# Performance work log

Measured on AMD Instinct MI355X. Metric: run time of the kernel, lower is better.

## Reference

```python
import jax, jax.numpy as jnp
import numpy as np

B = 256      # number of graphs
IN = 128     # input_dim
FD = 256     # feature_dim (dims[1])
HID = 256    # hidden_dim of attention block (dims[2])
OUT = 128    # final output dim (dims[3])
TXT = 512    # text_emb_dim

LENGTHS = np.asarray(128 + (np.arange(B) % 256), dtype=np.int64)  # ragged lens 128..383
N = int(LENGTHS.sum())  # 65408 total nodes
LMAX = int(LENGTHS.max())  # 383


def setup_inputs() -> dict:
    key = jax.random.key(0)
    ks = jax.random.split(key, 16)
    s = 0.02
    return {
        "input": jax.random.normal(ks[0], (N, IN), jnp.float32),
        "text_emb": jax.random.normal(ks[1], (B, TXT), jnp.float32),
        "repeat_list": jnp.asarray(LENGTHS),
        # layer 0: Linear(IN -> FD)
        "W0": jax.random.normal(ks[2], (IN, FD), jnp.float32) * s,
        "b0": jax.random.normal(ks[3], (FD,), jnp.float32) * s,
        # cross-attention block params
        "Wq": jax.random.normal(ks[4], (TXT, FD), jnp.float32) * s,
        "bq": jax.random.normal(ks[5], (FD,), jnp.float32) * s,
        "Wk": jax.random.normal(ks[6], (FD, FD), jnp.float32) * s,
        "bk": jax.random.normal(ks[7], (FD,), jnp.float32) * s,
        "Wv": jax.random.normal(ks[8], (FD, FD), jnp.float32) * s,
        "bv": jax.random.normal(ks[9], (FD,), jnp.float32) * s,
        "Wo": jax.random.normal(ks[10], (FD, HID), jnp.float32) * s,
        "bo": jax.random.normal(ks[11], (HID,), jnp.float32) * s,
        # layer 2: Linear(HID -> OUT), last layer (no activation)
        "W2": jax.random.normal(ks[12], (HID, OUT), jnp.float32) * s,
        "b2": jax.random.normal(ks[13], (OUT,), jnp.float32) * s,
    }


def _cross_attention(h, text_emb, repeat_list, Wq, bq, Wk, bk, Wv, bv, Wo, bo):
    # h: [N, FD] packed ragged node features; repeat_list: [B] lengths (constant ints)
    n = h.shape[0]
    b = repeat_list.shape[0]
    fd = h.shape[1]
    # pad ragged -> [B, LMAX, FD] (pad value 0) + validity mask
    seg = jnp.repeat(jnp.arange(b), repeat_list, total_repeat_length=n)  # [N] graph id
    offsets = jnp.cumsum(repeat_list) - repeat_list                      # [B] start of each graph
    pos = jnp.arange(n) - offsets[seg]                                   # [N] within-graph pos
    padded = jnp.zeros((b, LMAX, fd), h.dtype).at[seg, pos].set(h)
    valid = jnp.arange(LMAX)[None, :] < repeat_list[:, None]             # [B, L]

    q = text_emb @ Wq + bq                              # [B, FD]
    k = (padded @ Wk + bk) * valid[..., None]           # masked_fill(mask==0, 0)
    v = (padded @ Wv + bv) * valid[..., None]

    # query is broadcast identically over the padded-length axis, so each row of the
    # [L, L] score matrix is the same vector: scores[b, j] = q[b] . k[b, j]
    scores = jnp.einsum('bf,bjf->bj', q, k)             # [B, L]
    scores = jnp.where(valid, scores, -jnp.inf)         # mask invalid columns j
    p = jax.nn.softmax(scores, axis=-1)                 # [B, L]
    # output = attention^T @ value with identical rows => out[b,j,:] = p[b,j] * sum_i v[b,i,:]
    v_sum = v.sum(axis=1)                               # [B, FD] (padded rows already zero)
    out_pad = p[..., None] * v_sum[:, None, :]          # [B, L, FD]
    out_nodes = out_pad[seg, pos]                       # unpad-concat -> [N, FD]
    return out_nodes @ Wo + bo                          # [N, HID]


def reference(input, text_emb, repeat_list, W0, b0, Wq, bq, Wk, bk, Wv, bv, Wo, bo, W2, b2):
    h = jax.nn.relu(input @ W0 + b0)                                     # layer 0 + relu
    h = _cross_attention(h, text_emb, repeat_list, Wq, bq, Wk, bk, Wv, bv, Wo, bo)
    h = jax.nn.relu(h)                                                   # layer 1 + relu
    return h @ W2 + b2                                                   # layer 2 (last, no act)
```

## Files before the change

kernel.cpp:

```cpp
#include <hip/hip_runtime.h>
#include <math.h>

#define B_G   256
#define IN_D  128
#define FD    256
#define HID   256
#define OUT_D 128
#define TXT   512
#define XKS   136
#define ZKS   264

typedef short bf16x8 __attribute__((ext_vector_type(8)));
typedef float f32x4  __attribute__((ext_vector_type(4)));

__device__ __forceinline__ unsigned bf_rne(float x) {
    unsigned u = __float_as_uint(x);
    u += 0x7fffu + ((u >> 16) & 1u);
    return u >> 16;
}
__device__ __forceinline__ float bf_to_f(unsigned h) {
    return __uint_as_float(h << 16);
}
__device__ __forceinline__ void split2(float a0, float a1, unsigned& hp, unsigned& lp) {
    unsigned h0 = bf_rne(a0), h1 = bf_rne(a1);
    float r0 = a0 - bf_to_f(h0), r1 = a1 - bf_to_f(h1);
    hp = h0 | (h1 << 16);
    lp = bf_rne(r0) | (bf_rne(r1) << 16);
}

__global__ __launch_bounds__(256) void k_prepA(
    const float* __restrict__ text_emb, const float* __restrict__ Wq,
    const float* __restrict__ bq, const float* __restrict__ Wk,
    const float* __restrict__ W0, const float* __restrict__ W2,
    const int* __restrict__ lens,
    float* __restrict__ qk, int* __restrict__ offsets, float* __restrict__ hsum,
    unsigned short* __restrict__ W0sH, unsigned short* __restrict__ W0sL,
    unsigned short* __restrict__ W2sH, unsigned short* __restrict__ W2sL)
{
    int blk = blockIdx.x, t = threadIdx.x;
    __shared__ float te[TXT];
    __shared__ float q[FD];
    __shared__ int   sc[B_G];

    if (blk < 256) {
        int b = blk;
        hsum[b * FD + t] = 0.f;
        for (int i = t; i < TXT; i += 256) te[i] = text_emb[(size_t)b * TXT + i];
        __syncthreads();
        float acc = bq[t];
        for (int k = 0; k < TXT; k++) acc = fmaf(te[k], Wq[k * FD + t], acc);
        q[t] = acc;
        __syncthreads();
        float a2 = 0.f;
        for (int f = 0; f < FD; f++) a2 = fmaf(Wk[t * FD + f], q[f], a2);
        qk[b * FD + t] = a2;
    } else if (blk < 264) {
        int e = (blk - 256) * 256 + t;
        if (e < 1024) {
            int kc = e >> 8, c = e & 255;
            size_t base = (size_t)(kc * 256 + c) * 32;
            for (int kk = 0; kk < 32; kk++) {
                float v = W0[(size_t)(kc * 32 + kk) * FD + c];
                unsigned h = bf_rne(v);
                float r = v - bf_to_f(h);
                W0sH[base + kk] = (unsigned short)h;
                W0sL[base + kk] = (unsigned short)bf_rne(r);
            }
        } else {
            int e2 = e - 1024;
            int kc = e2 >> 7, c = e2 & 127;
            size_t base = (size_t)(kc * 128 + c) * 32;
            for (int kk = 0; kk < 32; kk++) {
                float v = W2[(size_t)(kc * 32 + kk) * OUT_D + c];
                unsigned h = bf_rne(v);
                float r = v - bf_to_f(h);
                W2sH[base + kk] = (unsigned short)h;
                W2sL[base + kk] = (unsigned short)bf_rne(r);
            }
        }
    } else {
        sc[t] = lens[t];
        __syncthreads();
        for (int d = 1; d < 256; d <<= 1) {
            int v = (t >= d) ? sc[t - d] : 0;
            __syncthreads();
            sc[t] += v;
            __syncthreads();
        }
        offsets[t + 1] = sc[t];
        if (t == 0) offsets[0] = 0;
    }
}

__global__ __launch_bounds__(256, 2) void k_l0_mfma(
    const float* __restrict__ X,
    const unsigned short* __restrict__ W0sH, const unsigned short* __restrict__ W0sL,
    const float* __restrict__ b0, const float* __restrict__ qk,
    const int* __restrict__ offsets,
    float* __restrict__ scores, float* __restrict__ hsum)
{
    int b = blockIdx.y;
    int off = offsets[b], len = offsets[b + 1] - off;
    int n0 = blockIdx.x * 64;
    if (n0 >= len) return;
    int nvalid = min(64, len - n0);

    __shared__ __align__(16) unsigned short XsH[64 * XKS], XsL[64 * XKS];
    __shared__ float qks[FD];
    __shared__ float bsh[FD];
    __shared__ float red[4][64];

    int tid = threadIdx.x;
    int lane = tid & 63, w = tid >> 6;
    int ln = lane & 15, quad = lane >> 4;

    qks[tid] = qk[b * FD + tid];
    bsh[tid] = b0[tid];

    {
        int node_s = tid >> 2, ks = (tid & 3) * 32;
        const float* Xr = X + (size_t)(off + n0 + node_s) * IN_D + ks;
        float xv[32];
        if (node_s < nvalid) {
#pragma unroll
            for (int q2 = 0; q2 < 8; q2++) {
                float4 v = ((const float4*)Xr)[q2];
                xv[q2 * 4 + 0] = v.x; xv[q2 * 4 + 1] = v.y;
                xv[q2 * 4 + 2] = v.z; xv[q2 * 4 + 3] = v.w;
            }
        } else {
#pragma unroll
            for (int q2 = 0; q2 < 32; q2++) xv[q2] = 0.f;
        }
#pragma unroll
        for (int g = 0; g < 4; g++) {
            uint4 hq, lq;
            split2(xv[g * 8 + 0], xv[g * 8 + 1], hq.x, lq.x);
            split2(xv[g * 8 + 2], xv[g * 8 + 3], hq.y, lq.y);
            split2(xv[g * 8 + 4], xv[g * 8 + 5], hq.z, lq.z);
            split2(xv[g * 8 + 6], xv[g * 8 + 7], hq.w, lq.w);
            *(uint4*)&XsH[node_s * XKS + ks + g * 8] = hq;
            *(uint4*)&XsL[node_s * XKS + ks + g * 8] = lq;
        }
    }
    __syncthreads();

    f32x4 acc[4][4] = {};
#pragma unroll
    for (int kc = 0; kc < 4; kc++) {
        bf16x8 AH[4], AL[4], BH[4], BL[4];
#pragma unroll
        for (int i = 0; i < 4; i++) {
            AH[i] = *(const bf16x8*)&XsH[(16 * i + ln) * XKS + kc * 32 + quad * 8];
            AL[i] = *(const bf16x8*)&XsL[(16 * i + ln) * XKS + kc * 32 + quad * 8];
        }
#pragma unroll
        for (int j = 0; j < 4; j++) {
            int c = 64 * w + 16 * j + ln;
            size_t base = (size_t)(kc * 256 + c) * 32 + quad * 8;
            BH[j] = *(const bf16x8*)&W0sH[base];
            BL[j] = *(const bf16x8*)&W0sL[base];
        }
#pragma unroll
        for (int i = 0; i < 4; i++)
#pragma unroll
            for (int j = 0; j < 4; j++) {
                acc[i][j] = __builtin_amdgcn_mfma_f32_16x16x32_bf16(AH[i], BH[j], acc[i][j], 0, 0, 0);
                acc[i][j] = __builtin_amdgcn_mfma_f32_16x16x32_bf16(AH[i], BL[j], acc[i][j], 0, 0, 0);
                acc[i][j] = __builtin_amdgcn_mfma_f32_16x16x32_bf16(AL[i], BH[j], acc[i][j], 0, 0, 0);
            }
    }

    float sp[4][4];
    float cs[4] = {0.f, 0.f, 0.f, 0.f};
#pragma unroll
    for (int i = 0; i < 4; i++)
#pragma unroll
        for (int r = 0; r < 4; r++) sp[i][r] = 0.f;

#pragma unroll
    for (int i = 0; i < 4; i++)
#pragma unroll
        for (int j = 0; j < 4; j++) {
            int c = 64 * w + 16 * j + ln;
            float bb = bsh[c], qv = qks[c];
#pragma unroll
            for (int r = 0; r < 4; r++) {
                int node = 16 * i + 4 * quad + r;
                float h = acc[i][j][r] + bb;
                h = (h > 0.f && node < nvalid) ? h : 0.f;
                sp[i][r] = fmaf(h, qv, sp[i][r]);
                cs[j] += h;
            }
        }
#pragma unroll
    for (int i = 0; i < 4; i++)
#pragma unroll
        for (int r = 0; r < 4; r++) {
            float s = sp[i][r];
            s += __shfl_xor(s, 1); s += __shfl_xor(s, 2);
            s += __shfl_xor(s, 4); s += __shfl_xor(s, 8);
            sp[i][r] = s;
        }
    if (ln == 0) {
#pragma unroll
        for (int i = 0; i < 4; i++)
#pragma unroll
            for (int r = 0; r < 4; r++)
                red[w][16 * i + 4 * quad + r] = sp[i][r];
    }
#pragma unroll
    for (int j = 0; j < 4; j++) {
        float s = cs[j];
        s += __shfl_xor(s, 16); s += __shfl_xor(s, 32);
        if (quad == 0) atomicAdd(&hsum[b * FD + 64 * w + 16 * j + ln], s);
    }
    __syncthreads();
    if (tid < 64 && tid < nvalid)
        scores[off + n0 + tid] = red[0][tid] + red[1][tid] + red[2][tid] + red[3][tid];
}

__global__ __launch_bounds__(1024) void k_graph(
    const float* __restrict__ scores, const float* __restrict__ hsum,
    const float* __restrict__ Wv, const float* __restrict__ bv,
    const float* __restrict__ Wo, const int* __restrict__ offsets,
    float* __restrict__ wvec, float* __restrict__ smax, float* __restrict__ dinv)
{
    int b = blockIdx.x, tid = threadIdx.x;
    int t = tid & 255, g = tid >> 8;
    int off = offsets[b], len = offsets[b + 1] - off;
    __shared__ float redm[16], reds[16];
    __shared__ float hs[FD], vs[FD];
    __shared__ float part[4][FD];

    float m = -INFINITY;
    for (int i = tid; i < len; i += 1024) m = fmaxf(m, scores[off + i]);
    for (int d = 1; d < 64; d <<= 1) m = fmaxf(m, __shfl_xor(m, d));
    if ((tid & 63) == 0) redm[tid >> 6] = m;
    __syncthreads();
    m = -INFINITY;
#pragma unroll
    for (int k = 0; k < 16; k++) m = fmaxf(m, redm[k]);

    float s = 0.f;
    for (int i = tid; i < len; i += 1024) s += expf(scores[off + i] - m);
    for (int d = 1; d < 64; d <<= 1) s += __shfl_xor(s, d);
    if ((tid & 63) == 0) reds[tid >> 6] = s;
    if (g == 0) hs[t] = hsum[b * FD + t];
    __syncthreads();
    s = 0.f;
#pragma unroll
    for (int k = 0; k < 16; k++) s += reds[k];

    float acc = (g == 0) ? (float)len * bv[t] : 0.f;
    for (int f = 64 * g; f < 64 * g + 64; f++) acc = fmaf(hs[f], Wv[f * FD + t], acc);
    part[g][t] = acc;
    __syncthreads();
    if (g == 0) vs[t] = part[0][t] + part[1][t] + part[2][t] + part[3][t];
    __syncthreads();
    float a2 = 0.f;
    for (int f = 64 * g; f < 64 * g + 64; f++) a2 = fmaf(vs[f], Wo[f * HID + t], a2);
    part[g][t] = a2;
    __syncthreads();
    if (g == 0) wvec[b * HID + t] = part[0][t] + part[1][t] + part[2][t] + part[3][t];
    if (tid == 0) { smax[b] = m; dinv[b] = 1.0f / s; }
}

__global__ __launch_bounds__(256, 2) void k_fin_mfma(
    const float* __restrict__ scores, const float* __restrict__ wvec,
    const float* __restrict__ bo,
    const unsigned short* __restrict__ W2sH, const unsigned short* __restrict__ W2sL,
    const float* __restrict__ b2, const float* __restrict__ smax,
    const float* __restrict__ dinv, const int* __restrict__ offsets,
    float* __restrict__ Y)
{
    int b = blockIdx.y;
    int off = offsets[b], len = offsets[b + 1] - off;
    int n0 = blockIdx.x * 64;
    if (n0 >= len) return;
    int nvalid = min(64, len - n0);

    int tid = threadIdx.x;
    int lane = tid & 63, w = tid >> 6;
    int ln = lane & 15, quad = lane >> 4;

    __shared__ __align__(16) unsigned short ZsH[64 * ZKS], ZsL[64 * ZKS];
    __shared__ float ps[64];
    __shared__ float wsh[HID];
    __shared__ float bosh[HID];
    __shared__ float b2sh[OUT_D];

    wsh[tid] = wvec[b * HID + tid];
    bosh[tid] = bo[tid];
    if (tid < OUT_D) b2sh[tid] = b2[tid];
    if (tid < 64) {
        float p = 0.f;
        if (tid < nvalid) p = expf(scores[off + n0 + tid] - smax[b]) * dinv[b];
        ps[tid] = p;
    }
    __syncthreads();

    {
        int node_s = tid >> 2, ks = (tid & 3) * 64;
        float pn = ps[node_s];
#pragma unroll
        for (int g = 0; g < 8; g++) {
            uint4 hq, lq;
            int kb = ks + g * 8;
            float z0, z1;
            z0 = fmaxf(fmaf(pn, wsh[kb + 0], bosh[kb + 0]), 0.f);
            z1 = fmaxf(fmaf(pn, wsh[kb + 1], bosh[kb + 1]), 0.f);
            split2(z0, z1, hq.x, lq.x);
            z0 = fmaxf(fmaf(pn, wsh[kb + 2], bosh[kb + 2]), 0.f);
            z1 = fmaxf(fmaf(pn, wsh[kb + 3], bosh[kb + 3]), 0.f);
            split2(z0, z1, hq.y, lq.y);
            z0 = fmaxf(fmaf(pn, wsh[kb + 4], bosh[kb + 4]), 0.f);
            z1 = fmaxf(fmaf(pn, wsh[kb + 5], bosh[kb + 5]), 0.f);
            split2(z0, z1, hq.z, lq.z);
            z0 = fmaxf(fmaf(pn, wsh[kb + 6], bosh[kb + 6]), 0.f);
            z1 = fmaxf(fmaf(pn, wsh[kb + 7], bosh[kb + 7]), 0.f);
            split2(z0, z1, hq.w, lq.w);
            *(uint4*)&ZsH[node_s * ZKS + kb] = hq;
            *(uint4*)&ZsL[node_s * ZKS + kb] = lq;
        }
    }
    __syncthreads();

    f32x4 acc[4][2] = {};
#pragma unroll
    for (int kc = 0; kc < 8; kc++) {
        bf16x8 AH[4], AL[4], BH[2], BL[2];
#pragma unroll
        for (int i = 0; i < 4; i++) {
            AH[i] = *(const bf16x8*)&ZsH[(16 * i + ln) * ZKS + kc * 32 + quad * 8];
            AL[i] = *(const bf16x8*)&ZsL[(16 * i + ln) * ZKS + kc * 32 + quad * 8];
        }
#pragma unroll
        for (int j = 0; j < 2; j++) {
            int c = 32 * w + 16 * j + ln;
            size_t base = (size_t)(kc * 128 + c) * 32 + quad * 8;
            BH[j] = *(const bf16x8*)&W2sH[base];
            BL[j] = *(const bf16x8*)&W2sL[base];
        }
#pragma unroll
        for (int i = 0; i < 4; i++)
#pragma unroll
            for (int j = 0; j < 2; j++) {
                acc[i][j] = __builtin_amdgcn_mfma_f32_16x16x32_bf16(AH[i], BH[j], acc[i][j], 0, 0, 0);
                acc[i][j] = __builtin_amdgcn_mfma_f32_16x16x32_bf16(AH[i], BL[j], acc[i][j], 0, 0, 0);
                acc[i][j] = __builtin_amdgcn_mfma_f32_16x16x32_bf16(AL[i], BH[j], acc[i][j], 0, 0, 0);
            }
    }

#pragma unroll
    for (int i = 0; i < 4; i++)
#pragma unroll
        for (int j = 0; j < 2; j++) {
            int c = 32 * w + 16 * j + ln;
            float bb = b2sh[c];
#pragma unroll
            for (int r = 0; r < 4; r++) {
                int node = 16 * i + 4 * quad + r;
                if (node < nvalid)
                    Y[(size_t)(off + n0 + node) * OUT_D + c] = acc[i][j][r] + bb;
            }
        }
}

extern "C" void kernel_launch(void* const* d_in, const int* in_sizes, int n_in,
                              void* d_out, int out_size, void* d_ws, size_t ws_size,
                              hipStream_t stream)
{
    const float* X        = (const float*)d_in[0];
    const float* text_emb = (const float*)d_in[1];
    const int*   lens     = (const int*)d_in[2];
    const float* W0       = (const float*)d_in[3];
    const float* b0       = (const float*)d_in[4];
    const float* Wq       = (const float*)d_in[5];
    const float* bq       = (const float*)d_in[6];
    const float* Wk       = (const float*)d_in[7];
    const float* Wv       = (const float*)d_in[9];
    const float* bv       = (const float*)d_in[10];
    const float* Wo       = (const float*)d_in[11];
    const float* bo       = (const float*)d_in[12];
    const float* W2       = (const float*)d_in[13];
    const float* b2       = (const float*)d_in[14];
    float* Y = (float*)d_out;

    char* base = (char*)d_ws;
    size_t o = 0;
    int*   offsets = (int*)(base + o);            o += 1088;
    float* qkbuf   = (float*)(base + o);          o += 262144;
    float* wvec    = (float*)(base + o);          o += 262144;
    float* smaxb   = (float*)(base + o);          o += 1024;
    float* dinvb   = (float*)(base + o);          o += 1024;
    float* hsum    = (float*)(base + o);          o += 262144;
    float* scores  = (float*)(base + o);          o += 262144;
    unsigned short* W0sH = (unsigned short*)(base + o); o += 65536;
    unsigned short* W0sL = (unsigned short*)(base + o); o += 65536;
    unsigned short* W2sH = (unsigned short*)(base + o); o += 65536;
    unsigned short* W2sL = (unsigned short*)(base + o); o += 65536;

    k_prepA<<<265, 256, 0, stream>>>(text_emb, Wq, bq, Wk, W0, W2, lens,
                                     qkbuf, offsets, hsum, W0sH, W0sL, W2sH, W2sL);
    k_l0_mfma<<<dim3(6, B_G), 256, 0, stream>>>(X, W0sH, W0sL, b0, qkbuf, offsets, scores, hsum);
    k_graph<<<B_G, 1024, 0, stream>>>(scores, hsum, Wv, bv, Wo, offsets, wvec, smaxb, dinvb);
    k_fin_mfma<<<dim3(6, B_G), 256, 0, stream>>>(scores, wvec, bo, W2sH, W2sL, b2, smaxb, dinvb, offsets, Y);
}
```

Before: 199.2 us.

## Replace final MFMA GEMM with sorted breakpoint walk of piecewise-linear ReLU output

Within a graph, each node's hidden vector is relu(p*w + bo) with a per-graph w, so the final layer output is piecewise linear in the scalar p. The new final kernel sorts the ReLU breakpoints (-bo/w), buckets nodes by p, and walks the merged sequence from both ends, updating running slope and intercept vectors to produce Y = A*p + C + b2. This removes the per-node 256x128 matmul and the bf16 split of W2, at the cost of a serial per-graph walk, a bitonic sort, and one block per graph, which lowers parallelism. Accumulating slope and intercept in float across many breakpoints may shift rounding relative to the direct product.

After: 222.2 us. +11.5%, slower.

```diff
diff --git a/kernel.cpp b/kernel.cpp
--- a/kernel.cpp
+++ b/kernel.cpp
@@ -8,7 +8,6 @@
 #define OUT_D 128
 #define TXT   512
 #define XKS   136
-#define ZKS   264
 
 typedef short bf16x8 __attribute__((ext_vector_type(8)));
 typedef float f32x4  __attribute__((ext_vector_type(4)));
@@ -31,11 +30,9 @@
 __global__ __launch_bounds__(256) void k_prepA(
     const float* __restrict__ text_emb, const float* __restrict__ Wq,
     const float* __restrict__ bq, const float* __restrict__ Wk,
-    const float* __restrict__ W0, const float* __restrict__ W2,
-    const int* __restrict__ lens,
+    const float* __restrict__ W0, const int* __restrict__ lens,
     float* __restrict__ qk, int* __restrict__ offsets, float* __restrict__ hsum,
-    unsigned short* __restrict__ W0sH, unsigned short* __restrict__ W0sL,
-    unsigned short* __restrict__ W2sH, unsigned short* __restrict__ W2sL)
+    unsigned short* __restrict__ W0sH, unsigned short* __restrict__ W0sL)
 {
     int blk = blockIdx.x, t = threadIdx.x;
     __shared__ float te[TXT];
@@ -54,29 +51,16 @@
         float a2 = 0.f;
         for (int f = 0; f < FD; f++) a2 = fmaf(Wk[t * FD + f], q[f], a2);
         qk[b * FD + t] = a2;
-    } else if (blk < 264) {
+    } else if (blk < 260) {
         int e = (blk - 256) * 256 + t;
-        if (e < 1024) {
-            int kc = e >> 8, c = e & 255;
-            size_t base = (size_t)(kc * 256 + c) * 32;
-            for (int kk = 0; kk < 32; kk++) {
-                float v = W0[(size_t)(kc * 32 + kk) * FD + c];
-                unsigned h = bf_rne(v);
-                float r = v - bf_to_f(h);
-                W0sH[base + kk] = (unsigned short)h;
-                W0sL[base + kk] = (unsigned short)bf_rne(r);
-            }
-        } else {
-            int e2 = e - 1024;
-            int kc = e2 >> 7, c = e2 & 127;
-            size_t base = (size_t)(kc * 128 + c) * 32;
-            for (int kk = 0; kk < 32; kk++) {
-                float v = W2[(size_t)(kc * 32 + kk) * OUT_D + c];
-                unsigned h = bf_rne(v);
-                float r = v - bf_to_f(h);
-                W2sH[base + kk] = (unsigned short)h;
-                W2sL[base + kk] = (unsigned short)bf_rne(r);
-            }
+        int kc = e >> 8, c = e & 255;
+        size_t base = (size_t)(kc * 256 + c) * 32;
+        for (int kk = 0; kk < 32; kk++) {
+            float v = W0[(size_t)(kc * 32 + kk) * FD + c];
+            unsigned h = bf_rne(v);
+            float r = v - bf_to_f(h);
+            W0sH[base + kk] = (unsigned short)h;
+            W0sL[base + kk] = (unsigned short)bf_rne(r);
         }
     } else {
         sc[t] = lens[t];
@@ -266,105 +250,208 @@
     if (tid == 0) { smax[b] = m; dinv[b] = 1.0f / s; }
 }
 
-__global__ __launch_bounds__(256, 2) void k_fin_mfma(
+__global__ __launch_bounds__(256) void k_fin_walk(
     const float* __restrict__ scores, const float* __restrict__ wvec,
-    const float* __restrict__ bo,
-    const unsigned short* __restrict__ W2sH, const unsigned short* __restrict__ W2sL,
+    const float* __restrict__ bo, const float* __restrict__ W2,
     const float* __restrict__ b2, const float* __restrict__ smax,
     const float* __restrict__ dinv, const int* __restrict__ offsets,
     float* __restrict__ Y)
 {
-    int b = blockIdx.y;
+    int b = blockIdx.x, tid = threadIdx.x;
     int off = offsets[b], len = offsets[b + 1] - off;
-    int n0 = blockIdx.x * 64;
-    if (n0 >= len) return;
-    int nvalid = min(64, len - n0);
-
-    int tid = threadIdx.x;
-    int lane = tid & 63, w = tid >> 6;
-    int ln = lane & 15, quad = lane >> 4;
-
-    __shared__ __align__(16) unsigned short ZsH[64 * ZKS], ZsL[64 * ZKS];
-    __shared__ float ps[64];
-    __shared__ float wsh[HID];
-    __shared__ float bosh[HID];
-    __shared__ float b2sh[OUT_D];
-
-    wsh[tid] = wvec[b * HID + tid];
-    bosh[tid] = bo[tid];
-    if (tid < OUT_D) b2sh[tid] = b2[tid];
-    if (tid < 64) {
-        float p = 0.f;
-        if (tid < nvalid) p = expf(scores[off + n0 + tid] - smax[b]) * dinv[b];
-        ps[tid] = p;
-    }
-    __syncthreads();
-
+
+    __shared__ __align__(16) float W2s[HID][OUT_D];
+    __shared__ __align__(16) char scratch[10496];
+    __shared__ float tS[HID], dwS[HID], dbS[HID];
+    __shared__ int   kS[HID];
+    __shared__ float wS[HID], boS[HID];
+    __shared__ int   cnt[HID + 1];
+    __shared__ int   startS[HID + 2];
+    __shared__ float ps_s[384];
+    __shared__ int   nidx_s[384], bkt[384];
+    __shared__ float AINIT[4][OUT_D];
+    __shared__ float b2s[OUT_D];
+
+    unsigned long long* ebuf = (unsigned long long*)scratch;
+    float* ptmp  = (float*)scratch;
+    int*   rtmp  = (int*)(scratch + 1536);
+    float4* part4 = (float4*)scratch;
+    float* opA = (float*)scratch;
+    float* opB = (float*)(scratch + 2624);
+    int*   opN = (int*)(scratch + 5248);
+    int*   opK = (int*)(scratch + 7872);
+
+    float m = smax[b], di = dinv[b];
+
+    float wreg = wvec[b * HID + tid];
+    float breg = bo[tid];
+    wS[tid] = wreg; boS[tid] = breg;
+    if (tid < OUT_D) b2s[tid] = b2[tid];
     {
-        int node_s = tid >> 2, ks = (tid & 3) * 64;
-        float pn = ps[node_s];
-#pragma unroll
-        for (int g = 0; g < 8; g++) {
-            uint4 hq, lq;
-            int kb = ks + g * 8;
-            float z0, z1;
-            z0 = fmaxf(fmaf(pn, wsh[kb + 0], bosh[kb + 0]), 0.f);
-            z1 = fmaxf(fmaf(pn, wsh[kb + 1], bosh[kb + 1]), 0.f);
-            split2(z0, z1, hq.x, lq.x);
-            z0 = fmaxf(fmaf(pn, wsh[kb + 2], bosh[kb + 2]), 0.f);
-            z1 = fmaxf(fmaf(pn, wsh[kb + 3], bosh[kb + 3]), 0.f);
-            split2(z0, z1, hq.y, lq.y);
-            z0 = fmaxf(fmaf(pn, wsh[kb + 4], bosh[kb + 4]), 0.f);
-            z1 = fmaxf(fmaf(pn, wsh[kb + 5], bosh[kb + 5]), 0.f);
-            split2(z0, z1, hq.z, lq.z);
-            z0 = fmaxf(fmaf(pn, wsh[kb + 6], bosh[kb + 6]), 0.f);
-            z1 = fmaxf(fmaf(pn, wsh[kb + 7], bosh[kb + 7]), 0.f);
-            split2(z0, z1, hq.w, lq.w);
-            *(uint4*)&ZsH[node_s * ZKS + kb] = hq;
-            *(uint4*)&ZsL[node_s * ZKS + kb] = lq;
-        }
-    }
-    __syncthreads();
-
-    f32x4 acc[4][2] = {};
-#pragma unroll
-    for (int kc = 0; kc < 8; kc++) {
-        bf16x8 AH[4], AL[4], BH[2], BL[2];
-#pragma unroll
-        for (int i = 0; i < 4; i++) {
-            AH[i] = *(const bf16x8*)&ZsH[(16 * i + ln) * ZKS + kc * 32 + quad * 8];
-            AL[i] = *(const bf16x8*)&ZsL[(16 * i + ln) * ZKS + kc * 32 + quad * 8];
-        }
-#pragma unroll
-        for (int j = 0; j < 2; j++) {
-            int c = 32 * w + 16 * j + ln;
-            size_t base = (size_t)(kc * 128 + c) * 32 + quad * 8;
-            BH[j] = *(const bf16x8*)&W2sH[base];
-            BL[j] = *(const bf16x8*)&W2sL[base];
-        }
-#pragma unroll
-        for (int i = 0; i < 4; i++)
-#pragma unroll
-            for (int j = 0; j < 2; j++) {
-                acc[i][j] = __builtin_amdgcn_mfma_f32_16x16x32_bf16(AH[i], BH[j], acc[i][j], 0, 0, 0);
-                acc[i][j] = __builtin_amdgcn_mfma_f32_16x16x32_bf16(AH[i], BL[j], acc[i][j], 0, 0, 0);
-                acc[i][j] = __builtin_amdgcn_mfma_f32_16x16x32_bf16(AL[i], BH[j], acc[i][j], 0, 0, 0);
-            }
-    }
-
-#pragma unroll
-    for (int i = 0; i < 4; i++)
-#pragma unroll
-        for (int j = 0; j < 2; j++) {
-            int c = 32 * w + 16 * j + ln;
-            float bb = b2sh[c];
-#pragma unroll
-            for (int r = 0; r < 4; r++) {
-                int node = 16 * i + 4 * quad + r;
-                if (node < nvalid)
-                    Y[(size_t)(off + n0 + node) * OUT_D + c] = acc[i][j][r] + bb;
-            }
-        }
+        const float4* gv = (const float4*)W2;
+        float4* lv = (float4*)&W2s[0][0];
+        for (int i = tid; i < HID * OUT_D / 4; i += 256) lv[i] = gv[i];
+    }
+
+    bool isev = (wreg > 0.f && breg < 0.f) || (wreg < 0.f && breg > 0.f);
+    float tk = isev ? (-breg / wreg) : INFINITY;
+    ebuf[tid] = ((unsigned long long)__float_as_uint(tk) << 32) | (unsigned)tid;
+    int nE = __syncthreads_count(isev);
+    __syncthreads();
+
+    for (int ksz = 2; ksz <= 256; ksz <<= 1) {
+        for (int js = ksz >> 1; js > 0; js >>= 1) {
+            int ixj = tid ^ js;
+            if (ixj > tid) {
+                unsigned long long a = ebuf[tid], bb2 = ebuf[ixj];
+                bool sw = ((tid & ksz) == 0) ? (a > bb2) : (a < bb2);
+                if (sw) { ebuf[tid] = bb2; ebuf[ixj] = a; }
+            }
+            __syncthreads();
+        }
+    }
+
+    {
+        unsigned long long e = ebuf[tid];
+        int k = (int)(unsigned)(e & 0xffffffffULL);
+        unsigned tb = (unsigned)(e >> 32);
+        bool real = (tb & 0x7f800000u) != 0x7f800000u;
+        tS[tid] = __uint_as_float(tb);
+        float wv = wS[k], bv = boS[k];
+        dwS[tid] = real ? fabsf(wv) : 0.f;
+        dbS[tid] = real ? -fabsf(bv) : 0.f;
+        kS[tid] = k;
+        cnt[tid] = 0;
+        if (tid == 0) cnt[256] = 0;
+    }
+    __syncthreads();
+
+    for (int n = tid; n < len; n += 256) {
+        float p = expf(scores[off + n] - m) * di;
+        int r = 0;
+#pragma unroll
+        for (int st = 128; st > 0; st >>= 1)
+            if (tS[r + st - 1] < p) r += st;
+        ptmp[n] = p; rtmp[n] = r;
+        atomicAdd(&cnt[r], 1);
+    }
+    __syncthreads();
+
+    for (int d = 1; d < 256; d <<= 1) {
+        int v = (tid >= d) ? cnt[tid - d] : 0;
+        __syncthreads();
+        cnt[tid] += v;
+        __syncthreads();
+    }
+    startS[tid + 1] = cnt[tid];
+    if (tid == 0) { startS[0] = 0; startS[257] = len; }
+    __syncthreads();
+
+    cnt[tid] = startS[tid];
+    if (tid == 0) cnt[256] = startS[256];
+    __syncthreads();
+    for (int n = tid; n < len; n += 256) {
+        int r = rtmp[n];
+        float p = ptmp[n];
+        int slot = atomicAdd(&cnt[r], 1);
+        ps_s[slot] = p; nidx_s[slot] = n; bkt[slot] = r;
+    }
+    __syncthreads();
+
+    {
+        int cI = tid & 127, hh = tid >> 7;
+        float A0 = 0.f, C0 = 0.f, AE = 0.f, CE = 0.f;
+        for (int k = hh * 128; k < hh * 128 + 128; ++k) {
+            float vv = W2s[k][cI];
+            float wv = wS[k], bv = boS[k];
+            bool ini = (bv > 0.f) || (bv == 0.f && wv > 0.f);
+            bool pos = (wv > 0.f);
+            A0 = fmaf(ini ? wv : 0.f, vv, A0);
+            C0 = fmaf(ini ? bv : 0.f, vv, C0);
+            AE = fmaf(pos ? wv : 0.f, vv, AE);
+            CE = fmaf((pos || (wv == 0.f && bv > 0.f)) ? bv : 0.f, vv, CE);
+        }
+        part4[hh * 128 + cI] = make_float4(A0, C0, AE, CE);
+    }
+    __syncthreads();
+    if (tid < 128) {
+        float4 x = part4[tid], y = part4[128 + tid];
+        AINIT[0][tid] = x.x + y.x;
+        AINIT[1][tid] = x.y + y.y;
+        AINIT[2][tid] = x.z + y.z;
+        AINIT[3][tid] = x.w + y.w;
+    }
+    __syncthreads();
+
+    int L = len + nE;
+    int Lpad = (L + 7) & ~7;
+    for (int s = tid; s < len; s += 256) {
+        int j = bkt[s];
+        int pos = s + j;
+        opA[pos] = ps_s[s]; opB[pos] = 0.f; opN[pos] = nidx_s[s]; opK[pos] = 0;
+    }
+    for (int j = tid; j < nE; j += 256) {
+        int pos = startS[j + 1] + j;
+        opA[pos] = dwS[j]; opB[pos] = dbS[j]; opN[pos] = -1; opK[pos] = kS[j];
+    }
+    for (int i = L + tid; i < Lpad + 8; i += 256) {
+        opA[i] = 0.f; opB[i] = 0.f; opN[i] = -1; opK[i] = 0;
+    }
+    __syncthreads();
+
+    {
+        int lane = tid & 63;
+        int c = ((tid >> 6) & 1) * 64 + lane;
+        float b2v = b2s[c];
+        float* Yb = Y + (size_t)off * OUT_D + c;
+        int P = (L >> 1) & ~7;
+        float rA[8], rB[8], rV[4]; int rN[8], rK[8];
+        float A, C;
+        if (tid < 128) {
+            A = AINIT[0][c]; C = AINIT[1][c];
+#pragma unroll
+            for (int u = 0; u < 8; ++u) { rA[u]=opA[u]; rB[u]=opB[u]; rN[u]=opN[u]; rK[u]=opK[u]; }
+#pragma unroll
+            for (int u = 0; u < 4; ++u) rV[u] = W2s[rK[u]][c];
+            for (int i0 = 0; i0 < P; i0 += 8) {
+#pragma unroll
+                for (int u = 0; u < 8; ++u) {
+                    int i = i0 + u;
+                    float aI = rA[u], bI = rB[u], vv = rV[u & 3];
+                    int nI = rN[u];
+                    rA[u] = opA[i + 8]; rB[u] = opB[i + 8];
+                    rN[u] = opN[i + 8]; rK[u] = opK[i + 8];
+                    int kpf = (u < 4) ? rK[u + 4] : rK[u - 4];
+                    rV[u & 3] = W2s[kpf][c];
+                    if (nI >= 0) Yb[(size_t)nI * OUT_D] = fmaf(aI, A, C) + b2v;
+                    else { A = fmaf(aI, vv, A); C = fmaf(bI, vv, C); }
+                }
+            }
+        } else {
+            A = AINIT[2][c]; C = AINIT[3][c];
+            int base = Lpad - 8;
+#pragma unroll
+            for (int u = 0; u < 8; ++u) { rA[u]=opA[base+u]; rB[u]=opB[base+u]; rN[u]=opN[base+u]; rK[u]=opK[base+u]; }
+#pragma unroll
+            for (int u = 0; u < 4; ++u) rV[u] = W2s[rK[u + 4]][c];
+            for (int i0 = base; i0 >= P; i0 -= 8) {
+#pragma unroll
+                for (int uu = 0; uu < 8; ++uu) {
+                    int u = 7 - uu;
+                    int i = i0 + u;
+                    float aI = rA[u], bI = rB[u], vv = rV[u & 3];
+                    int nI = rN[u];
+                    int ipf = i - 8;
+                    rA[u] = opA[ipf]; rB[u] = opB[ipf];
+                    rN[u] = opN[ipf]; rK[u] = opK[ipf];
+                    int kpf = (u >= 4) ? rK[u - 4] : rK[u + 4];
+                    rV[u & 3] = W2s[kpf][c];
+                    if (nI >= 0) Yb[(size_t)nI * OUT_D] = fmaf(aI, A, C) + b2v;
+                    else { A = fmaf(-aI, vv, A); C = fmaf(-bI, vv, C); }
+                }
+            }
+        }
+    }
 }
 
 extern "C" void kernel_launch(void* const* d_in, const int* in_sizes, int n_in,
@@ -398,12 +485,10 @@
     float* scores  = (float*)(base + o);          o += 262144;
     unsigned short* W0sH = (unsigned short*)(base + o); o += 65536;
     unsigned short* W0sL = (unsigned short*)(base + o); o += 65536;
-    unsigned short* W2sH = (unsigned short*)(base + o); o += 65536;
-    unsigned short* W2sL = (unsigned short*)(base + o); o += 65536;
-
-    k_prepA<<<265, 256, 0, stream>>>(text_emb, Wq, bq, Wk, W0, W2, lens,
-                                     qkbuf, offsets, hsum, W0sH, W0sL, W2sH, W2sL);
+
+    k_prepA<<<261, 256, 0, stream>>>(text_emb, Wq, bq, Wk, W0, lens,
+                                     qkbuf, offsets, hsum, W0sH, W0sL);
     k_l0_mfma<<<dim3(6, B_G), 256, 0, stream>>>(X, W0sH, W0sL, b0, qkbuf, offsets, scores, hsum);
     k_graph<<<B_G, 1024, 0, stream>>>(scores, hsum, Wv, bv, Wo, offsets, wvec, smaxb, dinvb);
-    k_fin_mfma<<<dim3(6, B_G), 256, 0, stream>>>(scores, wvec, bo, W2sH, W2sL, b2, smaxb, dinvb, offsets, Y);
-}
+    k_fin_walk<<<B_G, 256, 0, stream>>>(scores, wvec, bo, W2, b2, smaxb, dinvb, offsets, Y);
+}
```

## Replace final MFMA GEMM with sorted breakpoint walk over piecewise-linear ReLU

Applied to the files above, without the earlier changes.

Each node's hidden vector is relu(p*w + bo), which is piecewise linear in the scalar p. The final layer is therefore computed by sorting ReLU breakpoints and nodes by p and walking them in order while updating running A and C accumulators, so each output is a single fma instead of a 256-deep GEMM row. This removes the split-bf16 MFMA work and the W2 preprocessing. In exchange it adds sorting, scans, atomics and a sequential walk per segment, and it changes the floating-point summation order.

Result: no change. 202.3 us (+1.5%).

```diff
diff --git a/kernel.cpp b/kernel.cpp
--- a/kernel.cpp
+++ b/kernel.cpp
@@ -8,7 +8,6 @@
 #define OUT_D 128
 #define TXT   512
 #define XKS   136
-#define ZKS   264
 
 typedef short bf16x8 __attribute__((ext_vector_type(8)));
 typedef float f32x4  __attribute__((ext_vector_type(4)));
@@ -31,11 +30,9 @@
 __global__ __launch_bounds__(256) void k_prepA(
     const float* __restrict__ text_emb, const float* __restrict__ Wq,
     const float* __restrict__ bq, const float* __restrict__ Wk,
-    const float* __restrict__ W0, const float* __restrict__ W2,
-    const int* __restrict__ lens,
+    const float* __restrict__ W0, const int* __restrict__ lens,
     float* __restrict__ qk, int* __restrict__ offsets, float* __restrict__ hsum,
-    unsigned short* __restrict__ W0sH, unsigned short* __restrict__ W0sL,
-    unsigned short* __restrict__ W2sH, unsigned short* __restrict__ W2sL)
+    unsigned short* __restrict__ W0sH, unsigned short* __restrict__ W0sL)
 {
     int blk = blockIdx.x, t = threadIdx.x;
     __shared__ float te[TXT];
@@ -54,29 +51,16 @@
         float a2 = 0.f;
         for (int f = 0; f < FD; f++) a2 = fmaf(Wk[t * FD + f], q[f], a2);
         qk[b * FD + t] = a2;
-    } else if (blk < 264) {
+    } else if (blk < 260) {
         int e = (blk - 256) * 256 + t;
-        if (e < 1024) {
-            int kc = e >> 8, c = e & 255;
-            size_t base = (size_t)(kc * 256 + c) * 32;
-            for (int kk = 0; kk < 32; kk++) {
-                float v = W0[(size_t)(kc * 32 + kk) * FD + c];
-                unsigned h = bf_rne(v);
-                float r = v - bf_to_f(h);
-                W0sH[base + kk] = (unsigned short)h;
-                W0sL[base + kk] = (unsigned short)bf_rne(r);
-            }
-        } else {
-            int e2 = e - 1024;
-            int kc = e2 >> 7, c = e2 & 127;
-            size_t base = (size_t)(kc * 128 + c) * 32;
-            for (int kk = 0; kk < 32; kk++) {
-                float v = W2[(size_t)(kc * 32 + kk) * OUT_D + c];
-                unsigned h = bf_rne(v);
-                float r = v - bf_to_f(h);
-                W2sH[base + kk] = (unsigned short)h;
-                W2sL[base + kk] = (unsigned short)bf_rne(r);
-            }
+        int kc = e >> 8, c = e & 255;
+        size_t base = (size_t)(kc * 256 + c) * 32;
+        for (int kk = 0; kk < 32; kk++) {
+            float v = W0[(size_t)(kc * 32 + kk) * FD + c];
+            unsigned h = bf_rne(v);
+            float r = v - bf_to_f(h);
+            W0sH[base + kk] = (unsigned short)h;
+            W0sL[base + kk] = (unsigned short)bf_rne(r);
         }
     } else {
         sc[t] = lens[t];
@@ -266,105 +250,176 @@
     if (tid == 0) { smax[b] = m; dinv[b] = 1.0f / s; }
 }
 
-__global__ __launch_bounds__(256, 2) void k_fin_mfma(
+__global__ __launch_bounds__(1024) void k_fin_walk(
     const float* __restrict__ scores, const float* __restrict__ wvec,
-    const float* __restrict__ bo,
-    const unsigned short* __restrict__ W2sH, const unsigned short* __restrict__ W2sL,
+    const float* __restrict__ bo, const float* __restrict__ W2,
     const float* __restrict__ b2, const float* __restrict__ smax,
     const float* __restrict__ dinv, const int* __restrict__ offsets,
     float* __restrict__ Y)
 {
-    int b = blockIdx.y;
+    int b = blockIdx.x, tid = threadIdx.x;
     int off = offsets[b], len = offsets[b + 1] - off;
-    int n0 = blockIdx.x * 64;
-    if (n0 >= len) return;
-    int nvalid = min(64, len - n0);
-
-    int tid = threadIdx.x;
-    int lane = tid & 63, w = tid >> 6;
-    int ln = lane & 15, quad = lane >> 4;
-
-    __shared__ __align__(16) unsigned short ZsH[64 * ZKS], ZsL[64 * ZKS];
-    __shared__ float ps[64];
-    __shared__ float wsh[HID];
-    __shared__ float bosh[HID];
-    __shared__ float b2sh[OUT_D];
-
-    wsh[tid] = wvec[b * HID + tid];
-    bosh[tid] = bo[tid];
-    if (tid < OUT_D) b2sh[tid] = b2[tid];
+
+    __shared__ float tOrig[256];
+    __shared__ float tS[256], dwS[256], dbS[256];
+    __shared__ int   kS[256];
+    __shared__ float wS[256], boS[256];
+    __shared__ int   cnt[257], startS[257];
+    __shared__ float A0s[OUT_D], C0s[OUT_D], b2s[OUT_D];
+    __shared__ float segA[8][OUT_D], segC[8][OUT_D];
+    __shared__ __align__(16) char ops_raw[656 * 16];
+    float* opA = (float*)ops_raw;
+    float* opB = (float*)(ops_raw + 2624);
+    int*   opN = (int*)(ops_raw + 5248);
+    int*   opK = (int*)(ops_raw + 7872);
+
+    float m = smax[b], di = dinv[b];
+
+    bool real = false;
+    if (tid < 256) {
+        float wv = wvec[b * HID + tid];
+        float bv = bo[tid];
+        wS[tid] = wv; boS[tid] = bv;
+        bool isev = (wv > 0.f && bv < 0.f) || (wv < 0.f && bv > 0.f);
+        float tk = isev ? (-bv / wv) : INFINITY;
+        real = isev && (tk < INFINITY);
+        tOrig[tid] = real ? tk : INFINITY;
+        cnt[tid] = 0;
+        if (tid == 0) cnt[256] = 0;
+    }
+    if (tid < OUT_D) b2s[tid] = b2[tid];
+    __syncthreads();
+
+    if (tid < 256) {
+        float tk = tOrig[tid];
+        int r = 0;
+        for (int j = 0; j < 256; j++) {
+            float tj = tOrig[j];
+            r += (tj < tk || (tj == tk && j < tid)) ? 1 : 0;
+        }
+        tS[r] = tk;
+        kS[r] = tid;
+        float wv = wS[tid], bv = boS[tid];
+        dwS[r] = real ? fabsf(wv) : 0.f;
+        dbS[r] = real ? -fabsf(bv) : 0.f;
+    }
+    {
+        int q = tid >> 7, c = tid & 127;
+        float pa = 0.f, pc = 0.f;
+        for (int k = q * 32; k < q * 32 + 32; ++k) {
+            float v = W2[(size_t)k * OUT_D + c];
+            float wv = wS[k], bv = boS[k];
+            bool ini = (bv > 0.f) || (bv == 0.f && wv > 0.f);
+            pa = fmaf(ini ? wv : 0.f, v, pa);
+            pc = fmaf(ini ? bv : 0.f, v, pc);
+        }
+        segA[q][c] = pa; segC[q][c] = pc;
+    }
+    int nE = __syncthreads_count(real);
+
+    float p_n = 0.f; int r_n = 0;
+    if (tid < len) {
+        p_n = expf(scores[off + tid] - m) * di;
+        int r = 0;
+#pragma unroll
+        for (int st = 128; st > 0; st >>= 1)
+            if (tS[r + st - 1] < p_n) r += st;
+        r_n = r;
+        atomicAdd(&cnt[r], 1);
+    }
+    if (tid < OUT_D) {
+        float sa = 0.f, sc2 = 0.f;
+#pragma unroll
+        for (int q = 0; q < 8; q++) { sa += segA[q][tid]; sc2 += segC[q][tid]; }
+        A0s[tid] = sa; C0s[tid] = sc2;
+    }
+    __syncthreads();
+
     if (tid < 64) {
-        float p = 0.f;
-        if (tid < nvalid) p = expf(scores[off + n0 + tid] - smax[b]) * dinv[b];
-        ps[tid] = p;
-    }
-    __syncthreads();
-
+        int l = tid;
+        int v0 = cnt[4 * l], v1 = cnt[4 * l + 1], v2 = cnt[4 * l + 2], v3 = cnt[4 * l + 3];
+        int s0 = v0, s1 = s0 + v1, s2 = s1 + v2, s3 = s2 + v3;
+        int run = s3;
+#pragma unroll
+        for (int d = 1; d < 64; d <<= 1) {
+            int t2 = __shfl_up(run, d);
+            if (l >= d) run += t2;
+        }
+        int base = run - s3;
+        startS[4 * l + 0] = base;      cnt[4 * l + 0] = base;
+        startS[4 * l + 1] = base + s0; cnt[4 * l + 1] = base + s0;
+        startS[4 * l + 2] = base + s1; cnt[4 * l + 2] = base + s1;
+        startS[4 * l + 3] = base + s2; cnt[4 * l + 3] = base + s2;
+        if (l == 63) { startS[256] = base + s3; cnt[256] = base + s3; }
+    }
+    __syncthreads();
+
+    int L    = len + nE;
+    int Lpad = (L + 7) & ~7;
+    int Lseg = ((Lpad + 63) >> 6) << 3;
+
+    if (tid < len) {
+        int slot = atomicAdd(&cnt[r_n], 1);
+        int pos = slot + r_n;
+        opA[pos] = p_n; opB[pos] = 0.f; opN[pos] = tid; opK[pos] = 0;
+    }
+    if (tid < nE) {
+        int pos = startS[tid + 1] + tid;
+        opA[pos] = dwS[tid]; opB[pos] = dbS[tid]; opN[pos] = -1; opK[pos] = kS[tid];
+    }
+    for (int i = L + tid; i < 648; i += 1024) {
+        opA[i] = 0.f; opB[i] = 0.f; opN[i] = -1; opK[i] = 0;
+    }
+    __syncthreads();
+
+    int s = tid >> 7, c = tid & 127;
     {
-        int node_s = tid >> 2, ks = (tid & 3) * 64;
-        float pn = ps[node_s];
-#pragma unroll
-        for (int g = 0; g < 8; g++) {
-            uint4 hq, lq;
-            int kb = ks + g * 8;
-            float z0, z1;
-            z0 = fmaxf(fmaf(pn, wsh[kb + 0], bosh[kb + 0]), 0.f);
-            z1 = fmaxf(fmaf(pn, wsh[kb + 1], bosh[kb + 1]), 0.f);
-            split2(z0, z1, hq.x, lq.x);
-            z0 = fmaxf(fmaf(pn, wsh[kb + 2], bosh[kb + 2]), 0.f);
-            z1 = fmaxf(fmaf(pn, wsh[kb + 3], bosh[kb + 3]), 0.f);
-            split2(z0, z1, hq.y, lq.y);
-            z0 = fmaxf(fmaf(pn, wsh[kb + 4], bosh[kb + 4]), 0.f);
-            z1 = fmaxf(fmaf(pn, wsh[kb + 5], bosh[kb + 5]), 0.f);
-            split2(z0, z1, hq.z, lq.z);
-            z0 = fmaxf(fmaf(pn, wsh[kb + 6], bosh[kb + 6]), 0.f);
-            z1 = fmaxf(fmaf(pn, wsh[kb + 7], bosh[kb + 7]), 0.f);
-            split2(z0, z1, hq.w, lq.w);
-            *(uint4*)&ZsH[node_s * ZKS + kb] = hq;
-            *(uint4*)&ZsL[node_s * ZKS + kb] = lq;
-        }
-    }
-    __syncthreads();
-
-    f32x4 acc[4][2] = {};
-#pragma unroll
-    for (int kc = 0; kc < 8; kc++) {
-        bf16x8 AH[4], AL[4], BH[2], BL[2];
-#pragma unroll
-        for (int i = 0; i < 4; i++) {
-            AH[i] = *(const bf16x8*)&ZsH[(16 * i + ln) * ZKS + kc * 32 + quad * 8];
-            AL[i] = *(const bf16x8*)&ZsL[(16 * i + ln) * ZKS + kc * 32 + quad * 8];
-        }
-#pragma unroll
-        for (int j = 0; j < 2; j++) {
-            int c = 32 * w + 16 * j + ln;
-            size_t base = (size_t)(kc * 128 + c) * 32 + quad * 8;
-            BH[j] = *(const bf16x8*)&W2sH[base];
-            BL[j] = *(const bf16x8*)&W2sL[base];
-        }
-#pragma unroll
-        for (int i = 0; i < 4; i++)
-#pragma unroll
-            for (int j = 0; j < 2; j++) {
-                acc[i][j] = __builtin_amdgcn_mfma_f32_16x16x32_bf16(AH[i], BH[j], acc[i][j], 0, 0, 0);
-                acc[i][j] = __builtin_amdgcn_mfma_f32_16x16x32_bf16(AH[i], BL[j], acc[i][j], 0, 0, 0);
-                acc[i][j] = __builtin_amdgcn_mfma_f32_16x16x32_bf16(AL[i], BH[j], acc[i][j], 0, 0, 0);
+        int iBeg = s * Lseg, iEnd = iBeg + Lseg;
+        int lo = 0, hi = nE;
+        while (lo < hi) {
+            int mid = (lo + hi) >> 1;
+            if (startS[mid + 1] + mid < iBeg) lo = mid + 1; else hi = mid;
+        }
+        float dA = 0.f, dC = 0.f;
+        for (int j = lo; j < nE && (startS[j + 1] + j) < iEnd; ++j) {
+            float v = W2[(size_t)kS[j] * OUT_D + c];
+            dA = fmaf(dwS[j], v, dA);
+            dC = fmaf(dbS[j], v, dC);
+        }
+        segA[s][c] = dA; segC[s][c] = dC;
+    }
+    __syncthreads();
+
+    {
+        float A = A0s[c], C = C0s[c];
+        for (int s2 = 0; s2 < s; ++s2) { A += segA[s2][c]; C += segC[s2][c]; }
+        float b2v = b2s[c];
+        float* Yb = Y + (size_t)off * OUT_D + c;
+        int i0 = s * Lseg;
+
+        float rA[8], rB[8], rV[8]; int rN[8], rK[8];
+#pragma unroll
+        for (int u = 0; u < 8; ++u) {
+            rA[u] = opA[i0 + u]; rB[u] = opB[i0 + u];
+            rN[u] = opN[i0 + u]; rK[u] = opK[i0 + u];
+        }
+#pragma unroll
+        for (int u = 0; u < 8; ++u) rV[u] = W2[(size_t)rK[u] * OUT_D + c];
+
+        for (int i0w = i0; i0w < i0 + Lseg; i0w += 8) {
+#pragma unroll
+            for (int u = 0; u < 8; ++u) {
+                int i = i0w + u;
+                float aI = rA[u], bI = rB[u], vv = rV[u];
+                int nI = rN[u];
+                rA[u] = opA[i + 8]; rB[u] = opB[i + 8];
+                rN[u] = opN[i + 8]; rK[u] = opK[i + 8];
+                rV[u] = W2[(size_t)rK[u] * OUT_D + c];
+                if (nI >= 0) Yb[(size_t)nI * OUT_D] = fmaf(aI, A, C) + b2v;
+                else { A = fmaf(aI, vv, A); C = fmaf(bI, vv, C); }
             }
-    }
-
-#pragma unroll
-    for (int i = 0; i < 4; i++)
-#pragma unroll
-        for (int j = 0; j < 2; j++) {
-            int c = 32 * w + 16 * j + ln;
-            float bb = b2sh[c];
-#pragma unroll
-            for (int r = 0; r < 4; r++) {
-                int node = 16 * i + 4 * quad + r;
-                if (node < nvalid)
-                    Y[(size_t)(off + n0 + node) * OUT_D + c] = acc[i][j][r] + bb;
-            }
-        }
+        }
+    }
 }
 
 extern "C" void kernel_launch(void* const* d_in, const int* in_sizes, int n_in,
@@ -398,12 +453,10 @@
     float* scores  = (float*)(base + o);          o += 262144;
     unsigned short* W0sH = (unsigned short*)(base + o); o += 65536;
     unsigned short* W0sL = (unsigned short*)(base + o); o += 65536;
-    unsigned short* W2sH = (unsigned short*)(base + o); o += 65536;
-    unsigned short* W2sL = (unsigned short*)(base + o); o += 65536;
-
-    k_prepA<<<265, 256, 0, stream>>>(text_emb, Wq, bq, Wk, W0, W2, lens,
-                                     qkbuf, offsets, hsum, W0sH, W0sL, W2sH, W2sL);
+
+    k_prepA<<<261, 256, 0, stream>>>(text_emb, Wq, bq, Wk, W0, lens,
+                                     qkbuf, offsets, hsum, W0sH, W0sL);
     k_l0_mfma<<<dim3(6, B_G), 256, 0, stream>>>(X, W0sH, W0sL, b0, qkbuf, offsets, scores, hsum);
     k_graph<<<B_G, 1024, 0, stream>>>(scores, hsum, Wv, bv, Wo, offsets, wvec, smaxb, dinvb);
-    k_fin_mfma<<<dim3(6, B_G), 256, 0, stream>>>(scores, wvec, bo, W2sH, W2sL, b2, smaxb, dinvb, offsets, Y);
-}
+    k_fin_walk<<<B_G, 1024, 0, stream>>>(scores, wvec, bo, W2, b2, smaxb, dinvb, offsets, Y);
+}
```

## Raise occupancy of MFMA kernels by cutting registers and halving LDS tile

Applied to the files above, without the earlier changes.

Both MFMA kernels now declare launch bounds of four blocks per CU instead of two. In the layer-0 kernel, X is streamed in float4 pairs instead of a 32-float register array, and B fragments are loaded per column tile right before use rather than held all at once. In the final kernel, the K=256 staging buffer is split into two K=128 halves that reuse one smaller LDS tile, which adds an extra barrier per half. The goal is more resident waves to hide memory latency, at the risk of spills or less instruction-level overlap.

Result: no change. 201.0 us (+0.9%).

```diff
diff --git a/kernel.cpp b/kernel.cpp
--- a/kernel.cpp
+++ b/kernel.cpp
@@ -8,7 +8,6 @@
 #define OUT_D 128
 #define TXT   512
 #define XKS   136
-#define ZKS   264
 
 typedef short bf16x8 __attribute__((ext_vector_type(8)));
 typedef float f32x4  __attribute__((ext_vector_type(4)));
@@ -92,7 +91,7 @@
     }
 }
 
-__global__ __launch_bounds__(256, 2) void k_l0_mfma(
+__global__ __launch_bounds__(256, 4) void k_l0_mfma(
     const float* __restrict__ X,
     const unsigned short* __restrict__ W0sH, const unsigned short* __restrict__ W0sL,
     const float* __restrict__ b0, const float* __restrict__ qk,
@@ -119,26 +118,18 @@
 
     {
         int node_s = tid >> 2, ks = (tid & 3) * 32;
-        const float* Xr = X + (size_t)(off + n0 + node_s) * IN_D + ks;
-        float xv[32];
-        if (node_s < nvalid) {
-#pragma unroll
-            for (int q2 = 0; q2 < 8; q2++) {
-                float4 v = ((const float4*)Xr)[q2];
-                xv[q2 * 4 + 0] = v.x; xv[q2 * 4 + 1] = v.y;
-                xv[q2 * 4 + 2] = v.z; xv[q2 * 4 + 3] = v.w;
-            }
-        } else {
-#pragma unroll
-            for (int q2 = 0; q2 < 32; q2++) xv[q2] = 0.f;
-        }
+        const float4* Xr4 = (const float4*)(X + (size_t)(off + n0 + node_s) * IN_D + ks);
+        bool v = (node_s < nvalid);
 #pragma unroll
         for (int g = 0; g < 4; g++) {
+            float4 a, c4;
+            if (v) { a = Xr4[2 * g]; c4 = Xr4[2 * g + 1]; }
+            else   { a = make_float4(0.f, 0.f, 0.f, 0.f); c4 = a; }
             uint4 hq, lq;
-            split2(xv[g * 8 + 0], xv[g * 8 + 1], hq.x, lq.x);
-            split2(xv[g * 8 + 2], xv[g * 8 + 3], hq.y, lq.y);
-            split2(xv[g * 8 + 4], xv[g * 8 + 5], hq.z, lq.z);
-            split2(xv[g * 8 + 6], xv[g * 8 + 7], hq.w, lq.w);
+            split2(a.x,  a.y,  hq.x, lq.x);
+            split2(a.z,  a.w,  hq.y, lq.y);
+            split2(c4.x, c4.y, hq.z, lq.z);
+            split2(c4.z, c4.w, hq.w, lq.w);
             *(uint4*)&XsH[node_s * XKS + ks + g * 8] = hq;
             *(uint4*)&XsL[node_s * XKS + ks + g * 8] = lq;
         }
@@ -148,7 +139,7 @@
     f32x4 acc[4][4] = {};
 #pragma unroll
     for (int kc = 0; kc < 4; kc++) {
-        bf16x8 AH[4], AL[4], BH[4], BL[4];
+        bf16x8 AH[4], AL[4];
 #pragma unroll
         for (int i = 0; i < 4; i++) {
             AH[i] = *(const bf16x8*)&XsH[(16 * i + ln) * XKS + kc * 32 + quad * 8];
@@ -158,17 +149,15 @@
         for (int j = 0; j < 4; j++) {
             int c = 64 * w + 16 * j + ln;
             size_t base = (size_t)(kc * 256 + c) * 32 + quad * 8;
-            BH[j] = *(const bf16x8*)&W0sH[base];
-            BL[j] = *(const bf16x8*)&W0sL[base];
-        }
-#pragma unroll
-        for (int i = 0; i < 4; i++)
-#pragma unroll
-            for (int j = 0; j < 4; j++) {
-                acc[i][j] = __builtin_amdgcn_mfma_f32_16x16x32_bf16(AH[i], BH[j], acc[i][j], 0, 0, 0);
-                acc[i][j] = __builtin_amdgcn_mfma_f32_16x16x32_bf16(AH[i], BL[j], acc[i][j], 0, 0, 0);
-                acc[i][j] = __builtin_amdgcn_mfma_f32_16x16x32_bf16(AL[i], BH[j], acc[i][j], 0, 0, 0);
-            }
+            bf16x8 BH = *(const bf16x8*)&W0sH[base];
+            bf16x8 BL = *(const bf16x8*)&W0sL[base];
+#pragma unroll
+            for (int i = 0; i < 4; i++) {
+                acc[i][j] = __builtin_amdgcn_mfma_f32_16x16x32_bf16(AH[i], BH, acc[i][j], 0, 0, 0);
+                acc[i][j] = __builtin_amdgcn_mfma_f32_16x16x32_bf16(AH[i], BL, acc[i][j], 0, 0, 0);
+                acc[i][j] = __builtin_amdgcn_mfma_f32_16x16x32_bf16(AL[i], BH, acc[i][j], 0, 0, 0);
+            }
+        }
     }
 
     float sp[4][4];
@@ -266,7 +255,7 @@
     if (tid == 0) { smax[b] = m; dinv[b] = 1.0f / s; }
 }
 
-__global__ __launch_bounds__(256, 2) void k_fin_mfma(
+__global__ __launch_bounds__(256, 4) void k_fin_mfma(
     const float* __restrict__ scores, const float* __restrict__ wvec,
     const float* __restrict__ bo,
     const unsigned short* __restrict__ W2sH, const unsigned short* __restrict__ W2sL,
@@ -284,7 +273,7 @@
     int lane = tid & 63, w = tid >> 6;
     int ln = lane & 15, quad = lane >> 4;
 
-    __shared__ __align__(16) unsigned short ZsH[64 * ZKS], ZsL[64 * ZKS];
+    __shared__ __align__(16) unsigned short ZsH[64 * XKS], ZsL[64 * XKS];
     __shared__ float ps[64];
     __shared__ float wsh[HID];
     __shared__ float bosh[HID];
@@ -300,56 +289,60 @@
     }
     __syncthreads();
 
-    {
-        int node_s = tid >> 2, ks = (tid & 3) * 64;
-        float pn = ps[node_s];
-#pragma unroll
-        for (int g = 0; g < 8; g++) {
-            uint4 hq, lq;
-            int kb = ks + g * 8;
-            float z0, z1;
-            z0 = fmaxf(fmaf(pn, wsh[kb + 0], bosh[kb + 0]), 0.f);
-            z1 = fmaxf(fmaf(pn, wsh[kb + 1], bosh[kb + 1]), 0.f);
-            split2(z0, z1, hq.x, lq.x);
-            z0 = fmaxf(fmaf(pn, wsh[kb + 2], bosh[kb + 2]), 0.f);
-            z1 = fmaxf(fmaf(pn, wsh[kb + 3], bosh[kb + 3]), 0.f);
-            split2(z0, z1, hq.y, lq.y);
-            z0 = fmaxf(fmaf(pn, wsh[kb + 4], bosh[kb + 4]), 0.f);
-            z1 = fmaxf(fmaf(pn, wsh[kb + 5], bosh[kb + 5]), 0.f);
-            split2(z0, z1, hq.z, lq.z);
-            z0 = fmaxf(fmaf(pn, wsh[kb + 6], bosh[kb + 6]), 0.f);
-            z1 = fmaxf(fmaf(pn, wsh[kb + 7], bosh[kb + 7]), 0.f);
-            split2(z0, z1, hq.w, lq.w);
-            *(uint4*)&ZsH[node_s * ZKS + kb] = hq;
-            *(uint4*)&ZsL[node_s * ZKS + kb] = lq;
-        }
-    }
-    __syncthreads();
-
     f32x4 acc[4][2] = {};
-#pragma unroll
-    for (int kc = 0; kc < 8; kc++) {
-        bf16x8 AH[4], AL[4], BH[2], BL[2];
-#pragma unroll
-        for (int i = 0; i < 4; i++) {
-            AH[i] = *(const bf16x8*)&ZsH[(16 * i + ln) * ZKS + kc * 32 + quad * 8];
-            AL[i] = *(const bf16x8*)&ZsL[(16 * i + ln) * ZKS + kc * 32 + quad * 8];
-        }
-#pragma unroll
-        for (int j = 0; j < 2; j++) {
-            int c = 32 * w + 16 * j + ln;
-            size_t base = (size_t)(kc * 128 + c) * 32 + quad * 8;
-            BH[j] = *(const bf16x8*)&W2sH[base];
-            BL[j] = *(const bf16x8*)&W2sL[base];
-        }
-#pragma unroll
-        for (int i = 0; i < 4; i++)
+    int node_s = tid >> 2, ks = (tid & 3) * 32;
+
+#pragma unroll
+    for (int h = 0; h < 2; h++) {
+        if (h) __syncthreads();
+        {
+            float pn = ps[node_s];
+            int kg0 = h * 128 + ks;
+#pragma unroll
+            for (int g = 0; g < 4; g++) {
+                uint4 hq, lq;
+                int kb = kg0 + g * 8;
+                float z0, z1;
+                z0 = fmaxf(fmaf(pn, wsh[kb + 0], bosh[kb + 0]), 0.f);
+                z1 = fmaxf(fmaf(pn, wsh[kb + 1], bosh[kb + 1]), 0.f);
+                split2(z0, z1, hq.x, lq.x);
+                z0 = fmaxf(fmaf(pn, wsh[kb + 2], bosh[kb + 2]), 0.f);
+                z1 = fmaxf(fmaf(pn, wsh[kb + 3], bosh[kb + 3]), 0.f);
+                split2(z0, z1, hq.y, lq.y);
+                z0 = fmaxf(fmaf(pn, wsh[kb + 4], bosh[kb + 4]), 0.f);
+                z1 = fmaxf(fmaf(pn, wsh[kb + 5], bosh[kb + 5]), 0.f);
+                split2(z0, z1, hq.z, lq.z);
+                z0 = fmaxf(fmaf(pn, wsh[kb + 6], bosh[kb + 6]), 0.f);
+                z1 = fmaxf(fmaf(pn, wsh[kb + 7], bosh[kb + 7]), 0.f);
+                split2(z0, z1, hq.w, lq.w);
+                *(uint4*)&ZsH[node_s * XKS + ks + g * 8] = hq;
+                *(uint4*)&ZsL[node_s * XKS + ks + g * 8] = lq;
+            }
+        }
+        __syncthreads();
+
+#pragma unroll
+        for (int kc = 0; kc < 4; kc++) {
+            bf16x8 AH[4], AL[4];
+#pragma unroll
+            for (int i = 0; i < 4; i++) {
+                AH[i] = *(const bf16x8*)&ZsH[(16 * i + ln) * XKS + kc * 32 + quad * 8];
+                AL[i] = *(const bf16x8*)&ZsL[(16 * i + ln) * XKS + kc * 32 + quad * 8];
+            }
 #pragma unroll
             for (int j = 0; j < 2; j++) {
-                acc[i][j] = __builtin_amdgcn_mfma_f32_16x16x32_bf16(AH[i], BH[j], acc[i][j], 0, 0, 0);
-                acc[i][j] = __builtin_amdgcn_mfma_f32_16x16x32_bf16(AH[i], BL[j], acc[i][j], 0, 0, 0);
-                acc[i][j] = __builtin_amdgcn_mfma_f32_16x16x32_bf16(AL[i], BH[j], acc[i][j], 0, 0, 0);
-            }
+                int c = 32 * w + 16 * j + ln;
+                size_t base = (size_t)((h * 4 + kc) * 128 + c) * 32 + quad * 8;
+                bf16x8 BH = *(const bf16x8*)&W2sH[base];
+                bf16x8 BL = *(const bf16x8*)&W2sL[base];
+#pragma unroll
+                for (int i = 0; i < 4; i++) {
+                    acc[i][j] = __builtin_amdgcn_mfma_f32_16x16x32_bf16(AH[i], BH, acc[i][j], 0, 0, 0);
+                    acc[i][j] = __builtin_amdgcn_mfma_f32_16x16x32_bf16(AH[i], BL, acc[i][j], 0, 0, 0);
+                    acc[i][j] = __builtin_amdgcn_mfma_f32_16x16x32_bf16(AL[i], BH, acc[i][j], 0, 0, 0);
+                }
+            }
+        }
     }
 
 #pragma unroll
@@ -391,7 +384,7 @@
     size_t o = 0;
     int*   offsets = (int*)(base + o);            o += 1088;
     float* qkbuf   = (float*)(base + o);          o += 262144;
-    float* wvec    = (float*)(base + o);          o += 262144;
+    float* wvecb   = (float*)(base + o);          o += 262144;
     float* smaxb   = (float*)(base + o);          o += 1024;
     float* dinvb   = (float*)(base + o);          o += 1024;
     float* hsum    = (float*)(base + o);          o += 262144;
@@ -404,6 +397,6 @@
     k_prepA<<<265, 256, 0, stream>>>(text_emb, Wq, bq, Wk, W0, W2, lens,
                                      qkbuf, offsets, hsum, W0sH, W0sL, W2sH, W2sL);
     k_l0_mfma<<<dim3(6, B_G), 256, 0, stream>>>(X, W0sH, W0sL, b0, qkbuf, offsets, scores, hsum);
-    k_graph<<<B_G, 1024, 0, stream>>>(scores, hsum, Wv, bv, Wo, offsets, wvec, smaxb, dinvb);
-    k_fin_mfma<<<dim3(6, B_G), 256, 0, stream>>>(scores, wvec, bo, W2sH, W2sL, b2, smaxb, dinvb, offsets, Y);
-}
+    k_graph<<<B_G, 1024, 0, stream>>>(scores, hsum, Wv, bv, Wo, offsets, wvecb, smaxb, dinvb);
+    k_fin_mfma<<<dim3(6, B_G), 256, 0, stream>>>(scores, wvecb, bo, W2sH, W2sL, b2, smaxb, dinvb, offsets, Y);
+}
```
